# Optimization experiments

Hardware: AMD Instinct MI355X
Metric: run time of the kernel (lower is better)

## Reference

```python
import jax, jax.numpy as jnp
import numpy as np

B, T, R, A = 4, 40, 2000, 36864
H = W = 64
C = 256
PP = 7
RED = 16.0
NCLS = 21
NPOS = 64   # rois_per_image*B//4
NNEG = 192  # rois_per_image*B*3//4
DH = 1024

def _iou(b1, b2):
    # boxes are (top,left,bottom,right)
    t = jnp.maximum(b1[..., 0], b2[..., 0])
    l = jnp.maximum(b1[..., 1], b2[..., 1])
    b = jnp.minimum(b1[..., 2], b2[..., 2])
    r = jnp.minimum(b1[..., 3], b2[..., 3])
    inter = jnp.clip(b - t, 0.0) * jnp.clip(r - l, 0.0)
    a1 = (b1[..., 2] - b1[..., 0]) * (b1[..., 3] - b1[..., 1])
    a2 = (b2[..., 2] - b2[..., 0]) * (b2[..., 3] - b2[..., 1])
    return inter / (a1 + a2 - inter)

def _smooth_l1(p, t):
    d = jnp.abs(p - t)
    return jnp.mean(jnp.where(d < 1.0, 0.5 * d * d, d - 0.5))

def _roi_pool(fm, rois):
    # fm [B,C,H,W], rois [N,5] = (img_id, top,left,bottom,right) in feature-map coords
    fmt = jnp.transpose(fm, (0, 2, 3, 1))  # [B,H,W,C]
    n = rois[:, 0].astype(jnp.int32)[:, None, None]
    t, l, b, r = rois[:, 1], rois[:, 2], rois[:, 3], rois[:, 4]
    g = (jnp.arange(PP, dtype=fm.dtype) + 0.5) / PP
    ys = jnp.clip(t[:, None] + g * (b - t)[:, None], 0.0, H - 1.0)
    xs = jnp.clip(l[:, None] + g * (r - l)[:, None], 0.0, W - 1.0)
    y0 = jnp.floor(ys).astype(jnp.int32)
    x0 = jnp.floor(xs).astype(jnp.int32)
    y1 = jnp.minimum(y0 + 1, H - 1)
    x1 = jnp.minimum(x0 + 1, W - 1)
    wy = (ys - y0)[:, :, None, None]
    wx = (xs - x0)[:, None, :, None]
    def gat(yi, xi):
        return fmt[n, yi[:, :, None], xi[:, None, :], :]  # [N,PP,PP,C]
    v = (gat(y0, x0) * (1 - wy) * (1 - wx) + gat(y0, x1) * (1 - wy) * wx
         + gat(y1, x0) * wy * (1 - wx) + gat(y1, x1) * wy * wx)
    return v.reshape(v.shape[0], -1)  # [N, PP*PP*C]

def _forward(nms_reg, nms_cls, feature_maps, bboxes, classes, anchors, rpn_reg, rpn_cls, W1, b1, Wr, br, Wc, bc):
    # ---------------- RPN trainer: anchor/target matching ----------------
    iou_a = _iou(bboxes[:, :, None, :], anchors[None, None, :, :])   # [B,T,A]
    max_iou = jnp.max(iou_a, axis=1)                                  # [B,A]
    tidx = jnp.argmax(iou_a, axis=1)
    max_tgt = jnp.take_along_axis(bboxes, jnp.broadcast_to(tidx[:, :, None], (B, A, 4)), axis=1)
    mask = (max_iou > 0.5).reshape(-1)
    pos = jnp.nonzero(mask, size=128)[0]        # first 128 positives, flat order (matches cls[mask][:128])
    neg = jnp.nonzero(~mask, size=256 - B)[0]   # torch quirk: 256 - len(mask_matched) = 256 - B
    clsf = rpn_cls.reshape(-1)
    logits = jnp.concatenate([clsf[pos], clsf[neg]])
    lbl = jnp.concatenate([jnp.ones(128, dtype=logits.dtype), jnp.zeros(256 - B, dtype=logits.dtype)])
    rpn_cls_loss = jnp.mean(jnp.maximum(logits, 0) - logits * lbl + jnp.log1p(jnp.exp(-jnp.abs(logits))))
    anc_f = jnp.broadcast_to(anchors[None], (B, A, 4)).reshape(-1, 4)
    rpn_reg_loss = _smooth_l1(rpn_reg.reshape(-1, 4)[pos], max_tgt.reshape(-1, 4)[pos] - anc_f[pos]) / 4.0

    # ------------- RCNN trainer: proposal matching + sampling -------------
    iou_r = _iou(nms_reg[:, None, :, :], bboxes[:, :, None, :])  # [B,T,R]
    iou_m = jnp.max(iou_r, axis=1)                               # [B,R]
    ridx = jnp.argmax(iou_r, axis=1)
    iou_f = iou_m.reshape(-1)
    posr = jnp.nonzero(iou_f > 0.5, size=NPOS)[0]                # first NPOS positives, flat order
    negscore = jnp.where(iou_f <= 0.5, iou_f, -jnp.inf)
    negr = jax.lax.top_k(negscore, NNEG)[1]                      # negatives sorted by IoU descending
    cls_g = jnp.take_along_axis(classes, ridx, axis=1).reshape(-1)
    cls_s = jnp.concatenate([cls_g[posr], jnp.zeros(NNEG, dtype=cls_g.dtype)])
    imid = jnp.repeat(jnp.arange(B, dtype=nms_reg.dtype), R)
    nmsf = nms_reg.reshape(-1, 4)
    sel = jnp.concatenate([posr, negr])
    rois = jnp.concatenate([imid[sel][:, None], nmsf[sel]], axis=1)  # [256,5]
    feat = _roi_pool(feature_maps, rois)
    hmid = jax.nn.relu(feat @ W1 + b1)
    rreg = hmid @ Wr + br
    rcls = hmid @ Wc + bc
    logp = jax.nn.log_softmax(rcls, axis=-1)
    rcnn_cls_loss = -jnp.mean(jnp.take_along_axis(logp, cls_s[:, None], axis=1))
    posb = nmsf[posr]
    rounded = jnp.concatenate([jnp.floor(posb[:, :2] * RED), jnp.ceil(posb[:, 2:] * RED)], axis=1) / RED
    mb = jnp.take_along_axis(bboxes, jnp.broadcast_to(ridx[:, :, None], (B, R, 4)), axis=1).reshape(-1, 4)[posr]
    tgt = mb - rounded
    pr = rreg[:NPOS]
    rcnn_reg_loss = sum(_smooth_l1(pr[:, c], tgt[:, c]) for c in range(4)) / 4.0
    offset = sum(jnp.mean(jnp.abs(pr[:, c] - tgt[:, c])) for c in range(4)) / 4.0
    acc = jnp.mean((jnp.argmax(rcls[:NPOS], axis=-1) == cls_s[:NPOS]).astype(jnp.float32))
    return rpn_cls_loss, rpn_reg_loss, rcnn_cls_loss, rcnn_reg_loss, acc, offset

def _boxes(k, shape):
    k1, k2 = jax.random.split(k)
    c = jax.random.uniform(k1, shape + (2,), minval=10.0, maxval=54.0)
    h = jax.random.uniform(k2, shape + (2,), minval=3.0, maxval=8.0)
    return jnp.concatenate([c - h, c + h], axis=-1)  # (top,left,bottom,right)

def setup_inputs():
    key = jax.random.key(0)
    ks = jax.random.split(key, 13)
    base = _boxes(ks[0], (T,))
    shift = jax.random.uniform(ks[1], (B, T, 2), minval=-0.2, maxval=0.2)
    bboxes = base[None] + jnp.concatenate([shift, shift], axis=-1)  # guarantees >=128 RPN positives
    classes = jax.random.randint(ks[2], (B, T), 1, NCLS)
    anchors = _boxes(ks[3], (A,)).at[:T].set(base)
    nms_reg = _boxes(ks[4], (B, R))
    shift2 = jax.random.uniform(ks[5], (B, T, 2), minval=-0.1, maxval=0.1)
    nms_reg = nms_reg.at[:, :T].set(bboxes + jnp.concatenate([shift2, shift2], axis=-1))  # >=64 RCNN positives
    nms_cls = jax.random.normal(ks[6], (B, R))
    feature_maps = jax.random.normal(ks[7], (B, C, H, W))
    rpn_reg = 0.1 * jax.random.normal(ks[8], (B, A, 4))
    rpn_cls = jax.random.normal(ks[9], (B, A))
    D = PP * PP * C
    W1 = jax.random.normal(ks[10], (D, DH)) * float(1.0 / np.sqrt(D))
    b1 = jnp.zeros((DH,))
    Wr = jax.random.normal(ks[11], (DH, 4)) * float(1.0 / np.sqrt(DH))
    br = jnp.zeros((4,))
    Wc = jax.random.normal(ks[12], (DH, NCLS)) * float(1.0 / np.sqrt(DH))
    bc = jnp.zeros((NCLS,))
    return dict(nms_reg=nms_reg, nms_cls=nms_cls, feature_maps=feature_maps, bboxes=bboxes,
                classes=classes, anchors=anchors, rpn_reg=rpn_reg, rpn_cls=rpn_cls,
                W1=W1, b1=b1, Wr=Wr, br=br, Wc=Wc, bc=bc)

def reference(nms_reg, nms_cls, feature_maps, bboxes, classes, anchors, rpn_reg, rpn_cls, W1, b1, Wr, br, Wc, bc):
    return _forward(nms_reg, nms_cls, feature_maps, bboxes, classes, anchors, rpn_reg, rpn_cls, W1, b1, Wr, br, Wc, bc)
```

## Files before the change

kernel.cpp:

```cpp
#include <hip/hip_runtime.h>

typedef unsigned short u16;
typedef unsigned long long u64;

constexpr int cB = 4, cT = 40, cR = 2000, cA = 36864;
constexpr int cH = 64, cW = 64, cC = 256, cPP = 7;
constexpr int cNCLS = 21, cNPOS = 64, cNNEG = 192, cDH = 1024;
constexpr int cD = cPP * cPP * cC;
constexpr int cBA = cB * cA;
constexpr int cBR = cB * cR;
constexpr int NW64 = cBA / 64;
constexpr int SPLITS = 14;
constexpr int KCH = cD / SPLITS;
constexpr int BK = 64;
constexpr int NITER = KCH / BK;
constexpr unsigned POSKEY = 0x007FFFFFu;

constexpr size_t O_TIDX  = 0;
constexpr size_t O_MASKW = 589824;
constexpr size_t O_KEYS  = 608256;
constexpr size_t O_RIDXG = 640256;
constexpr size_t O_SEL   = 672256;
constexpr size_t O_CLS   = 673280;
constexpr size_t O_ROIS  = 674304;
constexpr size_t O_TGT   = 678400;
constexpr size_t O_FMT   = 1048576;
constexpr size_t O_FEAT  = O_FMT + 8388608;
constexpr size_t O_CPART = O_FEAT + 6422528;

__device__ __forceinline__ float b2f(u16 u) {
  return __uint_as_float(((unsigned)u) << 16);
}
__device__ __forceinline__ u16 f2b(float f) {
  unsigned x = __float_as_uint(f);
  unsigned r = x + 0x7FFFu + ((x >> 16) & 1u);
  return (u16)(r >> 16);
}
__device__ __forceinline__ unsigned f2key(float f) {
  unsigned b = __float_as_uint(f);
  return b ^ ((b & 0x80000000u) ? 0xFFFFFFFFu : 0x80000000u);
}

typedef __attribute__((ext_vector_type(8))) short short8;
typedef __attribute__((ext_vector_type(4))) float f32x4;

__global__ __launch_bounds__(256) void k_front(
    const float* __restrict__ bboxes, const float* __restrict__ anchors,
    const float* __restrict__ nms_reg, const float* __restrict__ fm,
    int* __restrict__ tidx, u64* __restrict__ maskw,
    unsigned* __restrict__ keys, int* __restrict__ ridxg,
    u16* __restrict__ fmt) {
  __shared__ float sfm[64 * 65];
  int bid = blockIdx.x;
  if (bid < 576) {
    float* sb = sfm;
    int b = bid / 144;
    if (threadIdx.x < cT * 4) sb[threadIdx.x] = bboxes[b * cT * 4 + threadIdx.x];
    __syncthreads();
    int i = bid * 256 + threadIdx.x;
    int a = i - b * cA;
    float4 av = ((const float4*)anchors)[a];
    float at = av.x, al = av.y, ab = av.z, ar = av.w;
    float area_a = (ab - at) * (ar - al);
    float best = -1.0f; int bi = 0;
    for (int t = 0; t < cT; ++t) {
      float bt = sb[t * 4], bl = sb[t * 4 + 1], bbv = sb[t * 4 + 2], brv = sb[t * 4 + 3];
      float ih = fmaxf(fminf(bbv, ab) - fmaxf(bt, at), 0.0f);
      float iw = fmaxf(fminf(brv, ar) - fmaxf(bl, al), 0.0f);
      float inter = ih * iw;
      float a1 = (bbv - bt) * (brv - bl);
      float iou = inter / (a1 + area_a - inter);
      if (iou > best) { best = iou; bi = t; }
    }
    tidx[i] = bi;
    u64 bal = __ballot(best > 0.5f);
    if ((threadIdx.x & 63) == 0) maskw[i >> 6] = bal;
  } else if (bid < 608) {
    float* sb = sfm;
    for (int j = threadIdx.x; j < cB * cT * 4; j += 256) sb[j] = bboxes[j];
    __syncthreads();
    int i = (bid - 576) * 256 + threadIdx.x;
    if (i >= cBR) return;
    int b = i / cR;
    float4 nv = ((const float4*)nms_reg)[i];
    float nt = nv.x, nl = nv.y, nb = nv.z, nr = nv.w;
    float area_n = (nb - nt) * (nr - nl);
    float best = -1.0f; int bi = 0;
    for (int t = 0; t < cT; ++t) {
      const float* bx = &sb[(b * cT + t) * 4];
      float ih = fmaxf(fminf(bx[2], nb) - fmaxf(bx[0], nt), 0.0f);
      float iw = fmaxf(fminf(bx[3], nr) - fmaxf(bx[1], nl), 0.0f);
      float inter = ih * iw;
      float a1 = (bx[2] - bx[0]) * (bx[3] - bx[1]);
      float iou = inter / (a1 + area_n - inter);
      if (iou > best) { best = iou; bi = t; }
    }
    keys[i] = (best <= 0.5f) ? f2key(best) : POSKEY;
    ridxg[i] = bi;
  } else {
    int f = bid - 608;
    int b = f >> 8;
    int c0 = ((f >> 6) & 3) * 64;
    int p0 = (f & 63) * 64;
    int t = threadIdx.x;
    int pL = (t & 15) * 4, cL = t >> 4;
    #pragma unroll
    for (int i = 0; i < 4; ++i) {
      int c = cL + i * 16;
      float4 v = *(const float4*)&fm[((size_t)b * cC + c0 + c) * (cH * cW) + p0 + pL];
      sfm[c * 65 + pL] = v.x; sfm[c * 65 + pL + 1] = v.y;
      sfm[c * 65 + pL + 2] = v.z; sfm[c * 65 + pL + 3] = v.w;
    }
    __syncthreads();
    int pW = t >> 2, cg = (t & 3) * 16;
    unsigned pk[8];
    #pragma unroll
    for (int j = 0; j < 8; ++j) {
      unsigned lo = f2b(sfm[(cg + 2 * j) * 65 + pW]);
      unsigned hi = f2b(sfm[(cg + 2 * j + 1) * 65 + pW]);
      pk[j] = lo | (hi << 16);
    }
    u16* dst = &fmt[((size_t)b * (cH * cW) + p0 + pW) * cC + c0 + cg];
    *(uint4*)dst = *(uint4*)&pk[0];
    *(uint4*)(dst + 8) = *(uint4*)&pk[4];
  }
}

__global__ __launch_bounds__(1024) void k_select(
    const u64* __restrict__ maskw, const int* __restrict__ tidx,
    const float* __restrict__ rpn_cls, const float* __restrict__ rpn_reg,
    const float* __restrict__ bboxes, const float* __restrict__ anchors,
    const unsigned* __restrict__ keysg, const int* __restrict__ ridxg,
    const float* __restrict__ nms_reg, const int* __restrict__ classes,
    int* __restrict__ sel, int* __restrict__ cls_s,
    float* __restrict__ rois, float* __restrict__ tgt,
    float* __restrict__ out) {
  __shared__ __align__(16) char smem[50688];
  __shared__ float s_scalF[2];
  __shared__ int s_scalI[3];
  int tid = threadIdx.x, lane = tid & 63, w = tid >> 6;
  u64 lmask = (1ULL << lane) - 1ULL;

  if (blockIdx.x == 0) {
    if (tid < 4) out[2 + tid] = 0.0f;
    u64* s_w   = (u64*)smem;
    int* s_pre = (int*)(smem + 18432);
    int* s_cw  = (int*)(smem + 19008);
    int* s_pos = (int*)(smem + 19584);
    int* s_neg = (int*)(smem + 20096);
    for (int k = tid; k < NW64; k += 1024) s_w[k] = maskw[k];
    if (tid < 128) s_pos[tid] = 0;
    if (tid < 252) s_neg[tid] = 0;
    if (tid == 0) { s_scalF[0] = 0.0f; s_scalF[1] = 0.0f; }
    __syncthreads();
    if (tid < 144) {
      int c = 0;
      #pragma unroll
      for (int k2 = 0; k2 < 16; ++k2) c += __popcll(s_w[tid * 16 + k2]);
      s_cw[tid] = c;
    }
    __syncthreads();
    if (tid == 0) {
      int run = 0;
      for (int ch = 0; ch < 144; ++ch) { s_pre[ch] = run; run += s_cw[ch]; }
    }
    __syncthreads();
    for (int ch = w; ch < 144; ch += 16) {
      int pbase = s_pre[ch];
      int nbase = ch * 1024 - pbase;
      if (pbase >= 128 && nbase >= 252) continue;
      int pc = 0;
      #pragma unroll
      for (int s2 = 0; s2 < 16; ++s2) {
        u64 word = s_w[ch * 16 + s2];
        bool m = (word >> lane) & 1ULL;
        int prefP = __popcll(word & lmask);
        int idx = ch * 1024 + s2 * 64 + lane;
        if (m) {
          int g = pbase + pc + prefP;
          if (g < 128) s_pos[g] = idx;
        } else {
          int g = nbase + (s2 * 64 + lane) - (pc + prefP);
          if (g < 252) s_neg[g] = idx;
        }
        pc += __popcll(word);
      }
    }
    __syncthreads();
    if (tid < 380) {
      int flat; float lbl;
      if (tid < 128) { flat = s_pos[tid]; lbl = 1.0f; }
      else           { flat = s_neg[tid - 128]; lbl = 0.0f; }
      float l = rpn_cls[flat];
      float term = fmaxf(l, 0.0f) - l * lbl + log1pf(expf(-fabsf(l)));
      atomicAdd(&s_scalF[0], term);
    }
    if (tid < 512) {
      int j = tid >> 2, c = tid & 3;
      int flat = s_pos[j];
      int b = flat / cA, a = flat - b * cA;
      int t = tidx[flat];
      float p = rpn_reg[flat * 4 + c];
      float tg = bboxes[(b * cT + t) * 4 + c] - anchors[a * 4 + c];
      float d = fabsf(p - tg);
      float sl = (d < 1.0f) ? 0.5f * d * d : d - 0.5f;
      atomicAdd(&s_scalF[1], sl);
    }
    __syncthreads();
    if (tid == 0) {
      out[0] = s_scalF[0] / 380.0f;
      out[1] = s_scalF[1] / 512.0f / 4.0f;
    }
  } else {
    unsigned* s_key = (unsigned*)smem;
    int* s_hist = (int*)(smem + 32000);
    int* s_pc   = (int*)(smem + 48384);
    int* s_wsum = (int*)(smem + 48896);
    int* s_wsuf = (int*)(smem + 48960);
    int* s_posr = (int*)(smem + 49024);
    int* s_negr = (int*)(smem + 49280);

    for (int i = tid; i < cBR; i += 1024) s_key[i] = keysg[i];
    if (tid < 64) s_posr[tid] = 0;
    __syncthreads();

    {
      int myv = 0; int mypre[8];
      #pragma unroll
      for (int p = 0; p < 8; ++p) {
        int i = p * 1024 + tid;
        bool v = (i < cBR) && (s_key[i] == POSKEY);
        u64 bal = __ballot(v);
        if (lane == 0) s_pc[p * 16 + w] = __popcll(bal);
        mypre[p] = __popcll(bal & lmask);
        myv |= v ? (1 << p) : 0;
      }
      __syncthreads();
      if (tid == 0) {
        int run = 0;
        for (int k = 0; k < 128; ++k) { int t = s_pc[k]; s_pc[k] = run; run += t; }
      }
      __syncthreads();
      #pragma unroll
      for (int p = 0; p < 8; ++p) {
        if (myv & (1 << p)) {
          int g = s_pc[p * 16 + w] + mypre[p];
          if (g < 64) s_posr[g] = p * 1024 + tid;
        }
      }
    }

    unsigned thr = 0; int G = 0;
    int need = cNNEG;
    #pragma unroll
    for (int lvl = 0; lvl < 3; ++lvl) {
      __syncthreads();
      #pragma unroll
      for (int k = 0; k < 4; ++k) s_hist[tid * 4 + k] = 0;
      __syncthreads();
      #pragma unroll
      for (int p = 0; p < 8; ++p) {
        int i = p * 1024 + tid;
        if (i < cBR) {
          unsigned key = s_key[i];
          int bkt = -1;
          if (lvl == 0) bkt = key >> 20;
          else if (lvl == 1) { if ((key >> 20) == (thr >> 20)) bkt = (key >> 8) & 0xFFF; }
          else { if ((key >> 8) == (thr >> 8)) bkt = (key & 0xFF) << 4; }
          if (bkt >= 0) atomicAdd(&s_hist[bkt], 1);
        }
      }
      __syncthreads();
      int local0 = s_hist[tid * 4 + 0], local1 = s_hist[tid * 4 + 1];
      int local2 = s_hist[tid * 4 + 2], local3 = s_hist[tid * 4 + 3];
      int lsum = local0 + local1 + local2 + local3;
      int x = lsum;
      #pragma unroll
      for (int off = 1; off < 64; off <<= 1) {
        int t = __shfl_down(x, off, 64);
        if (lane + off < 64) x += t;
      }
      if (lane == 0) s_wsum[w] = x;
      __syncthreads();
      if (tid == 0) {
        int run = 0;
        for (int wi = 15; wi >= 0; --wi) { s_wsuf[wi] = run; run += s_wsum[wi]; }
      }
      __syncthreads();
      int above = s_wsuf[w] + (x - lsum);
      int run = above;
      int loc[4] = {local3, local2, local1, local0};
      #pragma unroll
      for (int j = 0; j < 4; ++j) {
        int S = run + loc[j];
        if (run < need && S >= need) { s_scalI[0] = tid * 4 + (3 - j); s_scalI[1] = run; }
        run = S;
      }
      __syncthreads();
      int bS = s_scalI[0], ov = s_scalI[1];
      if (lvl == 0) thr = ((unsigned)bS) << 20;
      else if (lvl == 1) thr |= ((unsigned)bS) << 8;
      else thr |= ((unsigned)bS) >> 4;
      G += ov;
      need -= ov;
    }

    if (tid == 0) s_scalI[2] = 0;
    __syncthreads();
    #pragma unroll
    for (int p = 0; p < 8; ++p) {
      int i = p * 1024 + tid;
      if (i < cBR && s_key[i] > thr) {
        int slot = atomicAdd(&s_scalI[2], 1);
        s_negr[slot] = i;
      }
    }
    {
      __syncthreads();
      int myv = 0; int mypre[8];
      #pragma unroll
      for (int p = 0; p < 8; ++p) {
        int i = p * 1024 + tid;
        bool v = (i < cBR) && (s_key[i] == thr);
        u64 bal = __ballot(v);
        if (lane == 0) s_pc[p * 16 + w] = __popcll(bal);
        mypre[p] = __popcll(bal & lmask);
        myv |= v ? (1 << p) : 0;
      }
      __syncthreads();
      if (tid == 0) {
        int run = 0;
        for (int k = 0; k < 128; ++k) { int t = s_pc[k]; s_pc[k] = run; run += t; }
      }
      __syncthreads();
      #pragma unroll
      for (int p = 0; p < 8; ++p) {
        if (myv & (1 << p)) {
          int g = s_pc[p * 16 + w] + mypre[p];
          if (g < need) s_negr[G + g] = p * 1024 + tid;
        }
      }
    }
    __syncthreads();

    if (tid < 256) {
      int flat = (tid < 64) ? s_posr[tid] : s_negr[tid - 64];
      sel[tid] = flat;
      int b = flat / cR;
      #pragma unroll
      for (int c = 0; c < 4; ++c) rois[tid * 4 + c] = nms_reg[flat * 4 + c];
      cls_s[tid] = (tid < 64) ? classes[b * cT + ridxg[flat]] : 0;
      if (tid < 64) {
        int mt = ridxg[flat];
        #pragma unroll
        for (int c = 0; c < 4; ++c) {
          float v = nms_reg[flat * 4 + c];
          float rr = ((c < 2) ? floorf(v * 16.0f) : ceilf(v * 16.0f)) / 16.0f;
          float mbv = bboxes[(b * cT + mt) * 4 + c];
          tgt[tid * 4 + c] = mbv - rr;
        }
      }
    }
  }
}

__global__ void k_roi_pool(const u16* __restrict__ fmt, const float* __restrict__ rois,
                           const int* __restrict__ sel, u16* __restrict__ feat) {
  int j = blockIdx.x;
  int py = blockIdx.y;
  int c = threadIdx.x;
  int flat = sel[j];
  int n = flat / cR;
  float t = rois[j * 4 + 0], l = rois[j * 4 + 1];
  float bb = rois[j * 4 + 2], r = rois[j * 4 + 3];
  const u16* base = fmt + (size_t)n * (cH * cW) * cC;
  float gy = (py + 0.5f) / (float)cPP;
  float ys = fminf(fmaxf(t + gy * (bb - t), 0.0f), 63.0f);
  int y0 = (int)floorf(ys);
  int y1 = min(y0 + 1, 63);
  float wy = ys - (float)y0;
  #pragma unroll
  for (int px = 0; px < cPP; ++px) {
    float gx = (px + 0.5f) / (float)cPP;
    float xs = fminf(fmaxf(l + gx * (r - l), 0.0f), 63.0f);
    int x0 = (int)floorf(xs);
    int x1 = min(x0 + 1, 63);
    float wx = xs - (float)x0;
    float f00 = b2f(base[(y0 * cW + x0) * cC + c]);
    float f01 = b2f(base[(y0 * cW + x1) * cC + c]);
    float f10 = b2f(base[(y1 * cW + x0) * cC + c]);
    float f11 = b2f(base[(y1 * cW + x1) * cC + c]);
    float v = f00 * (1.0f - wy) * (1.0f - wx) + f01 * (1.0f - wy) * wx +
              f10 * wy * (1.0f - wx) + f11 * wy * wx;
    feat[((size_t)j * 49 + py * cPP + px) * cC + c] = f2b(v);
  }
}

__global__ __launch_bounds__(256) void k_gemm1(const u16* __restrict__ feat, const float* __restrict__ W1,
                                               float* __restrict__ Cpart) {
  __shared__ u16 As[2][64][64];
  __shared__ u16 Bs[2][32][64];
  int tid = threadIdx.x;
  int n0 = blockIdx.x * 32;
  int kb0 = blockIdx.y * KCH;
  int m0 = blockIdx.z * 64;
  int lane = tid & 63, w = tid >> 6;
  int r = lane & 15, q = lane >> 4;
  f32x4 acc0 = {}, acc1 = {};

  int am = tid >> 2;
  int ac0 = (tid & 3) * 2;
  int asw = am & 7;
  int ac0s = (ac0 ^ asw) * 8;
  int ac1s = ((ac0 + 1) ^ asw) * 8;
  int bn = tid & 31, bkc = tid >> 5;
  int bcs = (bkc ^ (bn & 7)) * 8;

  int rb = r & 7;
  int arow = w * 16 + r;
  int offK0 = ((0 * 4 + q) ^ rb) * 8;
  int offK1 = ((1 * 4 + q) ^ rb) * 8;

  const u16* ap = &feat[(size_t)(m0 + am) * cD + kb0 + ac0 * 8];
  const float* bp = &W1[(size_t)(kb0 + bkc * 8) * cDH + n0 + bn];

  uint4 ra0A, ra1A; float fA[8];
  uint4 ra0B, ra1B; float fB[8];

  ra0A = *(const uint4*)ap; ra1A = *(const uint4*)(ap + 8);
  #pragma unroll
  for (int j = 0; j < 8; ++j) fA[j] = bp[(size_t)j * cDH];
  ap += BK; bp += (size_t)BK * cDH;
  ra0B = *(const uint4*)ap; ra1B = *(const uint4*)(ap + 8);
  #pragma unroll
  for (int j = 0; j < 8; ++j) fB[j] = bp[(size_t)j * cDH];
  ap += BK; bp += (size_t)BK * cDH;
  *(uint4*)&As[0][am][ac0s] = ra0A;
  *(uint4*)&As[0][am][ac1s] = ra1A;
  {
    union { u16 u[8]; uint4 v; } pb;
    #pragma unroll
    for (int j = 0; j < 8; ++j) pb.u[j] = f2b(fA[j]);
    *(uint4*)&Bs[0][bn][bcs] = pb.v;
  }
  ra0A = *(const uint4*)ap; ra1A = *(const uint4*)(ap + 8);
  #pragma unroll
  for (int j = 0; j < 8; ++j) fA[j] = bp[(size_t)j * cDH];
  ap += BK; bp += (size_t)BK * cDH;
  __syncthreads();

  #pragma unroll
  for (int it = 0; it < NITER; it += 2) {
    *(uint4*)&As[1][am][ac0s] = ra0B;
    *(uint4*)&As[1][am][ac1s] = ra1B;
    {
      union { u16 u[8]; uint4 v; } pb;
      #pragma unroll
      for (int j = 0; j < 8; ++j) pb.u[j] = f2b(fB[j]);
      *(uint4*)&Bs[1][bn][bcs] = pb.v;
    }
    if (it + 3 < NITER) {
      ra0B = *(const uint4*)ap; ra1B = *(const uint4*)(ap + 8);
      #pragma unroll
      for (int j = 0; j < 8; ++j) fB[j] = bp[(size_t)j * cDH];
      ap += BK; bp += (size_t)BK * cDH;
    }
    {
      short8 a0 = *(const short8*)&As[0][arow][offK0];
      short8 b00 = *(const short8*)&Bs[0][r][offK0];
      short8 b10 = *(const short8*)&Bs[0][16 + r][offK0];
      acc0 = __builtin_amdgcn_mfma_f32_16x16x32_bf16(a0, b00, acc0, 0, 0, 0);
      acc1 = __builtin_amdgcn_mfma_f32_16x16x32_bf16(a0, b10, acc1, 0, 0, 0);
      short8 a1 = *(const short8*)&As[0][arow][offK1];
      short8 b01 = *(const short8*)&Bs[0][r][offK1];
      short8 b11 = *(const short8*)&Bs[0][16 + r][offK1];
      acc0 = __builtin_amdgcn_mfma_f32_16x16x32_bf16(a1, b01, acc0, 0, 0, 0);
      acc1 = __builtin_amdgcn_mfma_f32_16x16x32_bf16(a1, b11, acc1, 0, 0, 0);
    }
    __syncthreads();
    if (it + 2 < NITER) {
      *(uint4*)&As[0][am][ac0s] = ra0A;
      *(uint4*)&As[0][am][ac1s] = ra1A;
      {
        union { u16 u[8]; uint4 v; } pb;
        #pragma unroll
        for (int j = 0; j < 8; ++j) pb.u[j] = f2b(fA[j]);
        *(uint4*)&Bs[0][bn][bcs] = pb.v;
      }
      if (it + 4 < NITER) {
        ra0A = *(const uint4*)ap; ra1A = *(const uint4*)(ap + 8);
        #pragma unroll
        for (int j = 0; j < 8; ++j) fA[j] = bp[(size_t)j * cDH];
        ap += BK; bp += (size_t)BK * cDH;
      }
    }
    {
      short8 a0 = *(const short8*)&As[1][arow][offK0];
      short8 b00 = *(const short8*)&Bs[1][r][offK0];
      short8 b10 = *(const short8*)&Bs[1][16 + r][offK0];
      acc0 = __builtin_amdgcn_mfma_f32_16x16x32_bf16(a0, b00, acc0, 0, 0, 0);
      acc1 = __builtin_amdgcn_mfma_f32_16x16x32_bf16(a0, b10, acc1, 0, 0, 0);
      short8 a1 = *(const short8*)&As[1][arow][offK1];
      short8 b01 = *(const short8*)&Bs[1][r][offK1];
      short8 b11 = *(const short8*)&Bs[1][16 + r][offK1];
      acc0 = __builtin_amdgcn_mfma_f32_16x16x32_bf16(a1, b01, acc0, 0, 0, 0);
      acc1 = __builtin_amdgcn_mfma_f32_16x16x32_bf16(a1, b11, acc1, 0, 0, 0);
    }
    __syncthreads();
  }

  float* Cp = Cpart + (size_t)blockIdx.y * 256 * cDH;
  #pragma unroll
  for (int rg = 0; rg < 4; ++rg) {
    int row = m0 + w * 16 + q * 4 + rg;
    Cp[(size_t)row * cDH + n0 + r] = acc0[rg];
    Cp[(size_t)row * cDH + n0 + 16 + r] = acc1[rg];
  }
}

__global__ __launch_bounds__(256) void k_heads(
    const float* __restrict__ Cpart, const float* __restrict__ b1,
    const float* __restrict__ Wr, const float* __restrict__ br,
    const float* __restrict__ Wc, const float* __restrict__ bc,
    const int* __restrict__ cls_s, const float* __restrict__ tgt,
    float* __restrict__ out) {
  __shared__ float sacc[25];
  int row = blockIdx.x, tid = threadIdx.x, lane = tid & 63;
  if (tid < 25) sacc[tid] = 0.0f;
  __syncthreads();
  int k0 = tid * 4;
  float4 h = *(const float4*)&b1[k0];
  #pragma unroll
  for (int s = 0; s < SPLITS; ++s) {
    float4 c = *(const float4*)&Cpart[(size_t)s * 256 * cDH + (size_t)row * cDH + k0];
    h.x += c.x; h.y += c.y; h.z += c.z; h.w += c.w;
  }
  float hv[4] = {fmaxf(h.x, 0.f), fmaxf(h.y, 0.f), fmaxf(h.z, 0.f), fmaxf(h.w, 0.f)};
  float part[25];
  #pragma unroll
  for (int c = 0; c < 25; ++c) part[c] = 0.0f;
  #pragma unroll
  for (int j = 0; j < 4; ++j) {
    float4 wr = *(const float4*)&Wr[(k0 + j) * 4];
    part[0] += hv[j] * wr.x; part[1] += hv[j] * wr.y;
    part[2] += hv[j] * wr.z; part[3] += hv[j] * wr.w;
    const float* wc = &Wc[(k0 + j) * 21];
    #pragma unroll
    for (int c = 0; c < 21; ++c) part[4 + c] += hv[j] * wc[c];
  }
  #pragma unroll
  for (int off = 32; off; off >>= 1) {
    #pragma unroll
    for (int c = 0; c < 25; ++c) part[c] += __shfl_down(part[c], off, 64);
  }
  if (lane == 0) {
    #pragma unroll
    for (int c = 0; c < 25; ++c) atomicAdd(&sacc[c], part[c]);
  }
  __syncthreads();
  if (tid == 0) {
    int cls = cls_s[row];
    float m = -INFINITY;
    float vals[21];
    #pragma unroll
    for (int c = 0; c < 21; ++c) { vals[c] = sacc[4 + c] + bc[c]; m = fmaxf(m, vals[c]); }
    float sum = 0.0f;
    #pragma unroll
    for (int c = 0; c < 21; ++c) sum += expf(vals[c] - m);
    float lse = m + logf(sum);
    atomicAdd(&out[2], (lse - vals[cls]) * (1.0f / 256.0f));
    if (row < 64) {
      int am2 = 0; float bv = vals[0];
      #pragma unroll
      for (int c = 1; c < 21; ++c) if (vals[c] > bv) { bv = vals[c]; am2 = c; }
      if (am2 == cls) atomicAdd(&out[4], 1.0f / 64.0f);
    }
  }
  if (tid == 1 && row < 64) {
    float sl = 0.0f, of = 0.0f;
    #pragma unroll
    for (int c = 0; c < 4; ++c) {
      float d = fabsf((sacc[c] + br[c]) - tgt[row * 4 + c]);
      sl += (d < 1.0f) ? 0.5f * d * d : d - 0.5f;
      of += d;
    }
    atomicAdd(&out[3], sl * (1.0f / 256.0f));
    atomicAdd(&out[5], of * (1.0f / 256.0f));
  }
}

extern "C" void kernel_launch(void* const* d_in, const int* in_sizes, int n_in,
                              void* d_out, int out_size, void* d_ws, size_t ws_size,
                              hipStream_t stream) {
  const float* nms_reg = (const float*)d_in[0];
  const float* fm      = (const float*)d_in[2];
  const float* bboxes  = (const float*)d_in[3];
  const int*   classes = (const int*)d_in[4];
  const float* anchors = (const float*)d_in[5];
  const float* rpn_reg = (const float*)d_in[6];
  const float* rpn_cls = (const float*)d_in[7];
  const float* W1      = (const float*)d_in[8];
  const float* b1      = (const float*)d_in[9];
  const float* Wr      = (const float*)d_in[10];
  const float* br      = (const float*)d_in[11];
  const float* Wc      = (const float*)d_in[12];
  const float* bc      = (const float*)d_in[13];
  float* out = (float*)d_out;
  char* ws = (char*)d_ws;

  int*      tidx  = (int*)(ws + O_TIDX);
  u64*      maskw = (u64*)(ws + O_MASKW);
  unsigned* keys  = (unsigned*)(ws + O_KEYS);
  int*      ridxg = (int*)(ws + O_RIDXG);
  int*      sel   = (int*)(ws + O_SEL);
  int*      clss  = (int*)(ws + O_CLS);
  float*    rois  = (float*)(ws + O_ROIS);
  float*    tgt   = (float*)(ws + O_TGT);
  u16*      fmt   = (u16*)(ws + O_FMT);
  u16*      feat  = (u16*)(ws + O_FEAT);
  float*    Cpart = (float*)(ws + O_CPART);

  k_front<<<608 + 1024, 256, 0, stream>>>(bboxes, anchors, nms_reg, fm,
                                          tidx, maskw, keys, ridxg, fmt);
  k_select<<<2, 1024, 0, stream>>>(maskw, tidx, rpn_cls, rpn_reg, bboxes, anchors,
                                   keys, ridxg, nms_reg, classes, sel, clss, rois, tgt, out);
  k_roi_pool<<<dim3(256, cPP), 256, 0, stream>>>(fmt, rois, sel, feat);
  k_gemm1<<<dim3(32, SPLITS, 4), 256, 0, stream>>>(feat, W1, Cpart);
  k_heads<<<256, 256, 0, stream>>>(Cpart, b1, Wr, br, Wc, bc, clss, tgt, out);
}
```

Measured before the change: 193.1 us.

## Pre-transpose W1 to bf16 in front kernel and remap GEMM blocks for XCD locality

Adds 3136 blocks to the front kernel that convert W1 from fp32 to bf16 and transpose it to N-major layout into a new workspace buffer. The GEMM then loads B tiles as contiguous 16-byte bf16 vectors instead of eight strided fp32 scalars converted per iteration. The GEMM grid is also flattened and remapped so blocks sharing the same W1 column slice land on the same XCD across the four M tiles. The cost is an extra full pass over W1 (about 51 MB read, 25 MB written) inside the front kernel, though it can run alongside the other front work.

```diff
diff --git a/kernel.cpp b/kernel.cpp
--- a/kernel.cpp
+++ b/kernel.cpp
@@ -27,6 +27,7 @@
 constexpr size_t O_FMT   = 1048576;
 constexpr size_t O_FEAT  = O_FMT + 8388608;
 constexpr size_t O_CPART = O_FEAT + 6422528;
+constexpr size_t O_WT    = O_CPART + 14680064;
 
 __device__ __forceinline__ float b2f(u16 u) {
   return __uint_as_float(((unsigned)u) << 16);
@@ -47,9 +48,10 @@
 __global__ __launch_bounds__(256) void k_front(
     const float* __restrict__ bboxes, const float* __restrict__ anchors,
     const float* __restrict__ nms_reg, const float* __restrict__ fm,
+    const float* __restrict__ W1,
     int* __restrict__ tidx, u64* __restrict__ maskw,
     unsigned* __restrict__ keys, int* __restrict__ ridxg,
-    u16* __restrict__ fmt) {
+    u16* __restrict__ fmt, u16* __restrict__ wt) {
   __shared__ float sfm[64 * 65];
   int bid = blockIdx.x;
   if (bid < 576) {
@@ -97,7 +99,7 @@
     }
     keys[i] = (best <= 0.5f) ? f2key(best) : POSKEY;
     ridxg[i] = bi;
-  } else {
+  } else if (bid < 1632) {
     int f = bid - 608;
     int b = f >> 8;
     int c0 = ((f >> 6) & 3) * 64;
@@ -121,6 +123,31 @@
       pk[j] = lo | (hi << 16);
     }
     u16* dst = &fmt[((size_t)b * (cH * cW) + p0 + pW) * cC + c0 + cg];
+    *(uint4*)dst = *(uint4*)&pk[0];
+    *(uint4*)(dst + 8) = *(uint4*)&pk[4];
+  } else {
+    int f = bid - 1632;
+    int kt = f % 196, nt = f / 196;
+    int k0 = kt * 64, n0 = nt * 64;
+    int t = threadIdx.x;
+    int n4 = (t & 15) * 4, kL = t >> 4;
+    #pragma unroll
+    for (int i = 0; i < 4; ++i) {
+      int k = kL + i * 16;
+      float4 v = *(const float4*)&W1[(size_t)(k0 + k) * cDH + n0 + n4];
+      sfm[k * 65 + n4] = v.x; sfm[k * 65 + n4 + 1] = v.y;
+      sfm[k * 65 + n4 + 2] = v.z; sfm[k * 65 + n4 + 3] = v.w;
+    }
+    __syncthreads();
+    int n = t >> 2, kc = (t & 3) * 16;
+    unsigned pk[8];
+    #pragma unroll
+    for (int j = 0; j < 8; ++j) {
+      unsigned lo = f2b(sfm[(kc + 2 * j) * 65 + n]);
+      unsigned hi = f2b(sfm[(kc + 2 * j + 1) * 65 + n]);
+      pk[j] = lo | (hi << 16);
+    }
+    u16* dst = &wt[(size_t)(n0 + n) * cD + k0 + kc];
     *(uint4*)dst = *(uint4*)&pk[0];
     *(uint4*)(dst + 8) = *(uint4*)&pk[4];
   }
@@ -396,14 +423,19 @@
   }
 }
 
-__global__ __launch_bounds__(256) void k_gemm1(const u16* __restrict__ feat, const float* __restrict__ W1,
+__global__ __launch_bounds__(256) void k_gemm1(const u16* __restrict__ feat, const u16* __restrict__ Wt,
                                                float* __restrict__ Cpart) {
   __shared__ u16 As[2][64][64];
   __shared__ u16 Bs[2][32][64];
   int tid = threadIdx.x;
-  int n0 = blockIdx.x * 32;
-  int kb0 = blockIdx.y * KCH;
-  int m0 = blockIdx.z * 64;
+  int bid = blockIdx.x;
+  int xcd = bid & 7, jj = bid >> 3;
+  int gl = jj >> 2, m = jj & 3;
+  int g = gl * 8 + xcd;
+  int n0 = (g & 31) * 32;
+  int ksp = g >> 5;
+  int kb0 = ksp * KCH;
+  int m0 = m * 64;
   int lane = tid & 63, w = tid >> 6;
   int r = lane & 15, q = lane >> 4;
   f32x4 acc0 = {}, acc1 = {};
@@ -413,57 +445,37 @@
   int asw = am & 7;
   int ac0s = (ac0 ^ asw) * 8;
   int ac1s = ((ac0 + 1) ^ asw) * 8;
-  int bn = tid & 31, bkc = tid >> 5;
-  int bcs = (bkc ^ (bn & 7)) * 8;
+  int bn = tid >> 3, bc = tid & 7;
+  int bcs = (bc ^ (bn & 7)) * 8;
 
   int rb = r & 7;
   int arow = w * 16 + r;
-  int offK0 = ((0 * 4 + q) ^ rb) * 8;
-  int offK1 = ((1 * 4 + q) ^ rb) * 8;
+  int offK0 = (q ^ rb) * 8;
+  int offK1 = ((4 + q) ^ rb) * 8;
 
   const u16* ap = &feat[(size_t)(m0 + am) * cD + kb0 + ac0 * 8];
-  const float* bp = &W1[(size_t)(kb0 + bkc * 8) * cDH + n0 + bn];
-
-  uint4 ra0A, ra1A; float fA[8];
-  uint4 ra0B, ra1B; float fB[8];
-
-  ra0A = *(const uint4*)ap; ra1A = *(const uint4*)(ap + 8);
-  #pragma unroll
-  for (int j = 0; j < 8; ++j) fA[j] = bp[(size_t)j * cDH];
-  ap += BK; bp += (size_t)BK * cDH;
-  ra0B = *(const uint4*)ap; ra1B = *(const uint4*)(ap + 8);
-  #pragma unroll
-  for (int j = 0; j < 8; ++j) fB[j] = bp[(size_t)j * cDH];
-  ap += BK; bp += (size_t)BK * cDH;
-  *(uint4*)&As[0][am][ac0s] = ra0A;
-  *(uint4*)&As[0][am][ac1s] = ra1A;
-  {
-    union { u16 u[8]; uint4 v; } pb;
-    #pragma unroll
-    for (int j = 0; j < 8; ++j) pb.u[j] = f2b(fA[j]);
-    *(uint4*)&Bs[0][bn][bcs] = pb.v;
-  }
-  ra0A = *(const uint4*)ap; ra1A = *(const uint4*)(ap + 8);
-  #pragma unroll
-  for (int j = 0; j < 8; ++j) fA[j] = bp[(size_t)j * cDH];
-  ap += BK; bp += (size_t)BK * cDH;
+  const u16* bp = &Wt[(size_t)(n0 + bn) * cD + kb0 + bc * 8];
+
+  uint4 a0A, a1A, bA, a0B, a1B, bB;
+  a0A = *(const uint4*)ap; a1A = *(const uint4*)(ap + 8); bA = *(const uint4*)bp;
+  ap += BK; bp += BK;
+  a0B = *(const uint4*)ap; a1B = *(const uint4*)(ap + 8); bB = *(const uint4*)bp;
+  ap += BK; bp += BK;
+  *(uint4*)&As[0][am][ac0s] = a0A;
+  *(uint4*)&As[0][am][ac1s] = a1A;
+  *(uint4*)&Bs[0][bn][bcs] = bA;
+  a0A = *(const uint4*)ap; a1A = *(const uint4*)(ap + 8); bA = *(const uint4*)bp;
+  ap += BK; bp += BK;
   __syncthreads();
 
   #pragma unroll
   for (int it = 0; it < NITER; it += 2) {
-    *(uint4*)&As[1][am][ac0s] = ra0B;
-    *(uint4*)&As[1][am][ac1s] = ra1B;
-    {
-      union { u16 u[8]; uint4 v; } pb;
-      #pragma unroll
-      for (int j = 0; j < 8; ++j) pb.u[j] = f2b(fB[j]);
-      *(uint4*)&Bs[1][bn][bcs] = pb.v;
-    }
+    *(uint4*)&As[1][am][ac0s] = a0B;
+    *(uint4*)&As[1][am][ac1s] = a1B;
+    *(uint4*)&Bs[1][bn][bcs] = bB;
     if (it + 3 < NITER) {
-      ra0B = *(const uint4*)ap; ra1B = *(const uint4*)(ap + 8);
-      #pragma unroll
-      for (int j = 0; j < 8; ++j) fB[j] = bp[(size_t)j * cDH];
-      ap += BK; bp += (size_t)BK * cDH;
+      a0B = *(const uint4*)ap; a1B = *(const uint4*)(ap + 8); bB = *(const uint4*)bp;
+      ap += BK; bp += BK;
     }
     {
       short8 a0 = *(const short8*)&As[0][arow][offK0];
@@ -479,19 +491,12 @@
     }
     __syncthreads();
     if (it + 2 < NITER) {
-      *(uint4*)&As[0][am][ac0s] = ra0A;
-      *(uint4*)&As[0][am][ac1s] = ra1A;
-      {
-        union { u16 u[8]; uint4 v; } pb;
-        #pragma unroll
-        for (int j = 0; j < 8; ++j) pb.u[j] = f2b(fA[j]);
-        *(uint4*)&Bs[0][bn][bcs] = pb.v;
-      }
+      *(uint4*)&As[0][am][ac0s] = a0A;
+      *(uint4*)&As[0][am][ac1s] = a1A;
+      *(uint4*)&Bs[0][bn][bcs] = bA;
       if (it + 4 < NITER) {
-        ra0A = *(const uint4*)ap; ra1A = *(const uint4*)(ap + 8);
-        #pragma unroll
-        for (int j = 0; j < 8; ++j) fA[j] = bp[(size_t)j * cDH];
-        ap += BK; bp += (size_t)BK * cDH;
+        a0A = *(const uint4*)ap; a1A = *(const uint4*)(ap + 8); bA = *(const uint4*)bp;
+        ap += BK; bp += BK;
       }
     }
     {
@@ -509,7 +514,7 @@
     __syncthreads();
   }
 
-  float* Cp = Cpart + (size_t)blockIdx.y * 256 * cDH;
+  float* Cp = Cpart + (size_t)ksp * 256 * cDH;
   #pragma unroll
   for (int rg = 0; rg < 4; ++rg) {
     int row = m0 + w * 16 + q * 4 + rg;
@@ -619,12 +624,13 @@
   u16*      fmt   = (u16*)(ws + O_FMT);
   u16*      feat  = (u16*)(ws + O_FEAT);
   float*    Cpart = (float*)(ws + O_CPART);
-
-  k_front<<<608 + 1024, 256, 0, stream>>>(bboxes, anchors, nms_reg, fm,
-                                          tidx, maskw, keys, ridxg, fmt);
+  u16*      wt    = (u16*)(ws + O_WT);
+
+  k_front<<<608 + 1024 + 3136, 256, 0, stream>>>(bboxes, anchors, nms_reg, fm, W1,
+                                                 tidx, maskw, keys, ridxg, fmt, wt);
   k_select<<<2, 1024, 0, stream>>>(maskw, tidx, rpn_cls, rpn_reg, bboxes, anchors,
                                    keys, ridxg, nms_reg, classes, sel, clss, rois, tgt, out);
   k_roi_pool<<<dim3(256, cPP), 256, 0, stream>>>(fmt, rois, sel, feat);
-  k_gemm1<<<dim3(32, SPLITS, 4), 256, 0, stream>>>(feat, W1, Cpart);
+  k_gemm1<<<1792, 256, 0, stream>>>(feat, wt, Cpart);
   k_heads<<<256, 256, 0, stream>>>(Cpart, b1, Wr, br, Wc, bc, clss, tgt, out);
 }
```

Result: faster. 184.4 us, median of 2 (-4.5%).
